# Kernel tuning notes

Measured on AMD Instinct MI355X. Metric: run time of the kernel, lower is better.

The kernel has to match this reference:

```python
import jax, jax.numpy as jnp
import numpy as np

B, T, D, H = 256, 512, 512, 64


def setup_inputs() -> dict:
    key = jax.random.key(0)
    ks = jax.random.split(key, 9)
    s_ih = 1.0 / np.sqrt(H)
    inp = {
        "x": jax.random.normal(ks[0], (B, T, D), dtype=jnp.float32),
        # PyTorch LSTM params, gate order (i, f, g, o)
        "W_ih": jax.random.uniform(ks[1], (4 * H, D), jnp.float32, -s_ih, s_ih),
        "W_hh": jax.random.uniform(ks[2], (4 * H, H), jnp.float32, -s_ih, s_ih),
        "b_ih": jax.random.uniform(ks[3], (4 * H,), jnp.float32, -s_ih, s_ih),
        "b_hh": jax.random.uniform(ks[4], (4 * H,), jnp.float32, -s_ih, s_ih),
        "W1": jax.random.uniform(ks[5], (32, H), jnp.float32, -1 / np.sqrt(H), 1 / np.sqrt(H)),
        "b1": jax.random.uniform(ks[6], (32,), jnp.float32, -1 / np.sqrt(H), 1 / np.sqrt(H)),
        "W2": jax.random.uniform(ks[7], (3, 32), jnp.float32, -1 / np.sqrt(32), 1 / np.sqrt(32)),
        "b2": jax.random.uniform(ks[8], (3,), jnp.float32, -1 / np.sqrt(32), 1 / np.sqrt(32)),
    }
    return inp


def _lstm_mean(x, W_ih, W_hh, b_ih, b_hh):
    # Precompute input projection for all timesteps: [B,T,4H]
    x_proj = jnp.einsum('btd,gd->btg', x, W_ih) + b_ih + b_hh
    xs = jnp.swapaxes(x_proj, 0, 1)  # [T,B,4H]
    h0 = jnp.zeros((x.shape[0], H), x.dtype)
    c0 = jnp.zeros((x.shape[0], H), x.dtype)

    def step(carry, xt):
        h, c = carry
        gates = xt + h @ W_hh.T  # [B,4H]
        i, f, g, o = jnp.split(gates, 4, axis=-1)
        i = jax.nn.sigmoid(i)
        f = jax.nn.sigmoid(f)
        g = jnp.tanh(g)
        o = jax.nn.sigmoid(o)
        c = f * c + i * g
        h = o * jnp.tanh(c)
        return (h, c), h

    _, hs = jax.lax.scan(step, (h0, c0), xs)  # hs: [T,B,H]
    return jnp.mean(hs, axis=0)  # mean over time -> [B,H]


def reference(x, W_ih, W_hh, b_ih, b_hh, W1, b1, W2, b2):
    pooled = _lstm_mean(x, W_ih, W_hh, b_ih, b_hh)
    h = jax.nn.relu(pooled @ W1.T + b1)
    logits = h @ W2.T + b2
    return jax.nn.softmax(logits, axis=1)
```

## Files before the change

kernel.cpp:

```cpp
#include <hip/hip_runtime.h>
#include <hip/hip_bf16.h>

#define BB 256
#define TT 512
#define DD 512
#define HH 64
#define NG 256
#define MM (BB * TT)

#define BM 128
#define BN 256
#define BK 32
#define LDA 40
#define LDB 40
#define NKC (DD / BK)

typedef short short8 __attribute__((ext_vector_type(8)));
typedef short short4v __attribute__((ext_vector_type(4)));
typedef float f32x4 __attribute__((ext_vector_type(4)));

__device__ inline unsigned long long pack4bf16(float4 v) {
    __hip_bfloat162 lo = __float22bfloat162_rn(make_float2(v.x, v.y));
    __hip_bfloat162 hi = __float22bfloat162_rn(make_float2(v.z, v.w));
    unsigned lu, hu;
    __builtin_memcpy(&lu, &lo, 4);
    __builtin_memcpy(&hu, &hi, 4);
    return ((unsigned long long)hu << 32) | lu;
}

__device__ inline unsigned short f2bf(float f) {
    __hip_bfloat16 h = __float2bfloat16(f);
    unsigned short u;
    __builtin_memcpy(&u, &h, 2);
    return u;
}

__device__ inline float bf2f(unsigned short u) {
    unsigned x = ((unsigned)u) << 16;
    float f;
    __builtin_memcpy(&f, &x, 4);
    return f;
}

__global__ __launch_bounds__(512, 2) void gemm_xproj(
    const float* __restrict__ X,
    const float* __restrict__ W,
    const float* __restrict__ b_ih,
    const float* __restrict__ b_hh,
    unsigned short* __restrict__ XP)
{
    __shared__ unsigned short As[2][BM * LDA];
    __shared__ unsigned short Bs[2][BN * LDB];
    __shared__ float bias_s[NG];

    const int tid   = threadIdx.x;
    const int m_blk = blockIdx.x * BM;
    const int lane  = tid & 63;
    const int wv    = tid >> 6;
    const int wm    = wv & 1;
    const int wn    = wv >> 1;
    const int q     = lane >> 4;
    const int cn    = lane & 15;

    if (tid < NG) bias_s[tid] = b_ih[tid] + b_hh[tid];

    f32x4 acc[4][4];
#pragma unroll
    for (int i = 0; i < 4; ++i)
#pragma unroll
        for (int j = 0; j < 4; ++j) acc[i][j] = (f32x4)0.f;

    float4 a_r[2], b_r[4];

#define LOAD_TILE(KC)                                                                     \
    do {                                                                                  \
        const int kof = (KC) * BK;                                                        \
        _Pragma("unroll")                                                                 \
        for (int u = 0; u < 2; ++u) {                                                     \
            int c = tid + 512 * u;                                                        \
            a_r[u] = *(const float4*)(X + (size_t)(m_blk + (c >> 3)) * DD + kof + (c & 7) * 4); \
        }                                                                                 \
        _Pragma("unroll")                                                                 \
        for (int u = 0; u < 4; ++u) {                                                     \
            int c = tid + 512 * u;                                                        \
            b_r[u] = *(const float4*)(W + (size_t)(c >> 3) * DD + kof + (c & 7) * 4);     \
        }                                                                                 \
    } while (0)

    LOAD_TILE(0);

    for (int kc = 0; kc < NKC; ++kc) {
        const int p = kc & 1;
#pragma unroll
        for (int u = 0; u < 2; ++u) {
            int c = tid + 512 * u;
            *(unsigned long long*)&As[p][(c >> 3) * LDA + (c & 7) * 4] = pack4bf16(a_r[u]);
        }
#pragma unroll
        for (int u = 0; u < 4; ++u) {
            int c = tid + 512 * u;
            *(unsigned long long*)&Bs[p][(c >> 3) * LDB + (c & 7) * 4] = pack4bf16(b_r[u]);
        }
        if (kc + 1 < NKC) LOAD_TILE(kc + 1);
        __syncthreads();

        short8 af[4], bf[4];
#pragma unroll
        for (int i = 0; i < 4; ++i) {
            const unsigned short* pa = &As[p][(wm * 64 + i * 16 + cn) * LDA + q * 8];
            ((short4v*)&af[i])[0] = *(const short4v*)pa;
            ((short4v*)&af[i])[1] = *(const short4v*)(pa + 4);
        }
#pragma unroll
        for (int j = 0; j < 4; ++j) {
            const unsigned short* pb = &Bs[p][(wn * 64 + j * 16 + cn) * LDB + q * 8];
            ((short4v*)&bf[j])[0] = *(const short4v*)pb;
            ((short4v*)&bf[j])[1] = *(const short4v*)(pb + 4);
        }

#pragma unroll
        for (int i = 0; i < 4; ++i)
#pragma unroll
            for (int j = 0; j < 4; ++j)
                acc[i][j] = __builtin_amdgcn_mfma_f32_16x16x32_bf16(af[i], bf[j], acc[i][j], 0, 0, 0);
    }

#pragma unroll
    for (int j = 0; j < 4; ++j) {
        const int n   = wn * 64 + j * 16 + cn;
        const float bvv = bias_s[n];
#pragma unroll
        for (int i = 0; i < 4; ++i) {
            const int m0 = m_blk + wm * 64 + i * 16 + q * 4;
#pragma unroll
            for (int r = 0; r < 4; ++r)
                XP[(size_t)(m0 + r) * NG + n] = f2bf(acc[i][j][r] + bvv);
        }
    }
#undef LOAD_TILE
}

__global__ __launch_bounds__(256, 1) void lstm_rec(
    const unsigned short* __restrict__ XP,
    const float* __restrict__ Whh,
    float* __restrict__ pooled)
{
    const int b   = blockIdx.x;
    const int tid = threadIdx.x;
    const int wv  = tid >> 6;
    const int j   = tid & 63;

    float wrow[HH];
#pragma unroll
    for (int u = 0; u < HH / 4; ++u)
        ((float4*)wrow)[u] = ((const float4*)(Whh + (size_t)tid * HH))[u];

    __shared__ float gbuf[2][NG];

    float h = 0.f, c = 0.f, hsum = 0.f;
    const unsigned short* xp = XP + (size_t)b * TT * NG + tid;

    unsigned short xr[4];
#pragma unroll
    for (int u = 0; u < 4; ++u) xr[u] = xp[(size_t)u * NG];

    for (int t0 = 0; t0 < TT; t0 += 4) {
#pragma unroll
        for (int u = 0; u < 4; ++u) {
            const int t = t0 + u;
            float a0 = bf2f(xr[u]), a1 = 0.f, a2 = 0.f, a3 = 0.f;
            xr[u] = xp[(size_t)((t + 4) & (TT - 1)) * NG];

            const int hb = __float_as_int(h);
#pragma unroll
            for (int kb = 0; kb < HH; kb += 4) {
                float h0 = __int_as_float(__builtin_amdgcn_readlane(hb, kb + 0));
                float h1 = __int_as_float(__builtin_amdgcn_readlane(hb, kb + 1));
                float h2 = __int_as_float(__builtin_amdgcn_readlane(hb, kb + 2));
                float h3 = __int_as_float(__builtin_amdgcn_readlane(hb, kb + 3));
                a0 = fmaf(wrow[kb + 0], h0, a0);
                a1 = fmaf(wrow[kb + 1], h1, a1);
                a2 = fmaf(wrow[kb + 2], h2, a2);
                a3 = fmaf(wrow[kb + 3], h3, a3);
            }
            const float acc = (a0 + a1) + (a2 + a3);

            float a;
            if (wv == 2) {
                a = 2.f / (1.f + __expf(-2.f * acc)) - 1.f;
            } else {
                a = 1.f / (1.f + __expf(-acc));
            }
            const int p = t & 1;
            gbuf[p][tid] = a;
            __syncthreads();
            const float iv = gbuf[p][j];
            const float fv = gbuf[p][64 + j];
            const float gv = gbuf[p][128 + j];
            const float ov = gbuf[p][192 + j];
            c = fmaf(fv, c, iv * gv);
            const float th = 2.f / (1.f + __expf(-2.f * c)) - 1.f;
            h = ov * th;
            hsum += h;
        }
    }

    if (tid < HH) pooled[(size_t)b * HH + j] = hsum * (1.f / (float)TT);
}

__global__ __launch_bounds__(256) void head_kernel(
    const float* __restrict__ pooled,
    const float* __restrict__ W1,
    const float* __restrict__ b1,
    const float* __restrict__ W2,
    const float* __restrict__ b2,
    float* __restrict__ out)
{
    __shared__ float W1s[32 * HH];
    __shared__ float W2s[3 * 32];
    __shared__ float b1s[32];
    __shared__ float b2s[3];

    const int tid = threadIdx.x;
    for (int i = tid; i < 32 * HH; i += 256) W1s[i] = W1[i];
    if (tid < 96) W2s[tid] = W2[tid];
    if (tid < 32) b1s[tid] = b1[tid];
    if (tid < 3)  b2s[tid] = b2[tid];
    __syncthreads();

    float p[HH];
    const float4* p4 = (const float4*)(pooled + (size_t)tid * HH);
#pragma unroll
    for (int q = 0; q < HH / 4; ++q) ((float4*)p)[q] = p4[q];

    float hbuf[32];
#pragma unroll
    for (int k = 0; k < 32; ++k) {
        float s = b1s[k];
        const float* wr = &W1s[k * HH];
#pragma unroll
        for (int jj = 0; jj < HH; ++jj) s += p[jj] * wr[jj];
        hbuf[k] = s > 0.f ? s : 0.f;
    }

    float lg[3];
#pragma unroll
    for (int cc = 0; cc < 3; ++cc) {
        float s = b2s[cc];
        const float* wr = &W2s[cc * 32];
#pragma unroll
        for (int k = 0; k < 32; ++k) s += hbuf[k] * wr[k];
        lg[cc] = s;
    }

    float mx = fmaxf(lg[0], fmaxf(lg[1], lg[2]));
    float e0 = __expf(lg[0] - mx);
    float e1 = __expf(lg[1] - mx);
    float e2 = __expf(lg[2] - mx);
    float inv = 1.f / (e0 + e1 + e2);
    out[tid * 3 + 0] = e0 * inv;
    out[tid * 3 + 1] = e1 * inv;
    out[tid * 3 + 2] = e2 * inv;
}

extern "C" void kernel_launch(void* const* d_in, const int* in_sizes, int n_in,
                              void* d_out, int out_size, void* d_ws, size_t ws_size,
                              hipStream_t stream) {
    const float* x    = (const float*)d_in[0];
    const float* W_ih = (const float*)d_in[1];
    const float* W_hh = (const float*)d_in[2];
    const float* b_ih = (const float*)d_in[3];
    const float* b_hh = (const float*)d_in[4];
    const float* W1   = (const float*)d_in[5];
    const float* b1   = (const float*)d_in[6];
    const float* W2   = (const float*)d_in[7];
    const float* b2   = (const float*)d_in[8];
    float* out = (float*)d_out;

    unsigned short* XP = (unsigned short*)d_ws;
    float* pooled = (float*)((char*)d_ws + (size_t)MM * NG * sizeof(unsigned short));

    gemm_xproj<<<dim3(MM / BM), 512, 0, stream>>>(x, W_ih, b_ih, b_hh, XP);
    lstm_rec<<<dim3(BB), 256, 0, stream>>>(XP, W_hh, pooled);
    head_kernel<<<dim3(1), 256, 0, stream>>>(pooled, W1, b1, W2, b2, out);
}
```

Baseline: 640.4 us.

## Run LSTM recurrence in a single wavefront per batch with all gates per lane

The recurrence kernel now uses one 64-lane wavefront per batch row instead of four. Each lane holds all four gate rows of W_hh in registers (256 floats) and computes i, f, g, o itself, which removes the shared-memory gate exchange and the per-step __syncthreads. In exchange each lane does four times the FMAs per step and register pressure rises sharply, which risks spilling. Empty asm statements pin the weights in VGPRs, and the x_proj prefetch depth drops to two steps.

```diff
diff --git a/kernel.cpp b/kernel.cpp
--- a/kernel.cpp
+++ b/kernel.cpp
@@ -24,6 +24,7 @@
     __hip_bfloat162 hi = __float22bfloat162_rn(make_float2(v.z, v.w));
     unsigned lu, hu;
     __builtin_memcpy(&lu, &lo, 4);
+    __builtin_memcpy(&hu, &hu, 0);
     __builtin_memcpy(&hu, &hi, 4);
     return ((unsigned long long)hu << 32) | lu;
 }
@@ -140,72 +141,96 @@
 #undef LOAD_TILE
 }
 
-__global__ __launch_bounds__(256, 1) void lstm_rec(
+__global__ __launch_bounds__(64, 1) void lstm_rec(
     const unsigned short* __restrict__ XP,
     const float* __restrict__ Whh,
     float* __restrict__ pooled)
 {
-    const int b   = blockIdx.x;
-    const int tid = threadIdx.x;
-    const int wv  = tid >> 6;
-    const int j   = tid & 63;
-
-    float wrow[HH];
-#pragma unroll
-    for (int u = 0; u < HH / 4; ++u)
-        ((float4*)wrow)[u] = ((const float4*)(Whh + (size_t)tid * HH))[u];
-
-    __shared__ float gbuf[2][NG];
+    const int b = blockIdx.x;
+    const int j = threadIdx.x & 63;
+
+    const f32x4* Wiv = (const f32x4*)(Whh + (size_t)j * HH);
+    const f32x4* Wfv = (const f32x4*)(Whh + (size_t)(HH + j) * HH);
+    const f32x4* Wgv = (const f32x4*)(Whh + (size_t)(2 * HH + j) * HH);
+    const f32x4* Wov = (const f32x4*)(Whh + (size_t)(3 * HH + j) * HH);
+
+#define WL16(P, S)                                                        \
+    f32x4 P##0 = (S)[0],  P##1 = (S)[1],  P##2 = (S)[2],  P##3 = (S)[3],  \
+          P##4 = (S)[4],  P##5 = (S)[5],  P##6 = (S)[6],  P##7 = (S)[7],  \
+          P##8 = (S)[8],  P##9 = (S)[9],  P##10 = (S)[10], P##11 = (S)[11],\
+          P##12 = (S)[12], P##13 = (S)[13], P##14 = (S)[14], P##15 = (S)[15];
+    WL16(wi, Wiv)
+    WL16(wf, Wfv)
+    WL16(wg, Wgv)
+    WL16(wo, Wov)
+#undef WL16
+
+#define PIN16(P)                                                          \
+    asm volatile("" : "+v"(P##0), "+v"(P##1), "+v"(P##2),  "+v"(P##3),    \
+                      "+v"(P##4), "+v"(P##5), "+v"(P##6),  "+v"(P##7),    \
+                      "+v"(P##8), "+v"(P##9), "+v"(P##10), "+v"(P##11),   \
+                      "+v"(P##12), "+v"(P##13), "+v"(P##14), "+v"(P##15));
 
     float h = 0.f, c = 0.f, hsum = 0.f;
-    const unsigned short* xp = XP + (size_t)b * TT * NG + tid;
-
-    unsigned short xr[4];
-#pragma unroll
-    for (int u = 0; u < 4; ++u) xr[u] = xp[(size_t)u * NG];
-
-    for (int t0 = 0; t0 < TT; t0 += 4) {
-#pragma unroll
-        for (int u = 0; u < 4; ++u) {
-            const int t = t0 + u;
-            float a0 = bf2f(xr[u]), a1 = 0.f, a2 = 0.f, a3 = 0.f;
-            xr[u] = xp[(size_t)((t + 4) & (TT - 1)) * NG];
-
-            const int hb = __float_as_int(h);
-#pragma unroll
-            for (int kb = 0; kb < HH; kb += 4) {
-                float h0 = __int_as_float(__builtin_amdgcn_readlane(hb, kb + 0));
-                float h1 = __int_as_float(__builtin_amdgcn_readlane(hb, kb + 1));
-                float h2 = __int_as_float(__builtin_amdgcn_readlane(hb, kb + 2));
-                float h3 = __int_as_float(__builtin_amdgcn_readlane(hb, kb + 3));
-                a0 = fmaf(wrow[kb + 0], h0, a0);
-                a1 = fmaf(wrow[kb + 1], h1, a1);
-                a2 = fmaf(wrow[kb + 2], h2, a2);
-                a3 = fmaf(wrow[kb + 3], h3, a3);
-            }
-            const float acc = (a0 + a1) + (a2 + a3);
-
-            float a;
-            if (wv == 2) {
-                a = 2.f / (1.f + __expf(-2.f * acc)) - 1.f;
-            } else {
-                a = 1.f / (1.f + __expf(-acc));
-            }
-            const int p = t & 1;
-            gbuf[p][tid] = a;
-            __syncthreads();
-            const float iv = gbuf[p][j];
-            const float fv = gbuf[p][64 + j];
-            const float gv = gbuf[p][128 + j];
-            const float ov = gbuf[p][192 + j];
-            c = fmaf(fv, c, iv * gv);
-            const float th = 2.f / (1.f + __expf(-2.f * c)) - 1.f;
-            h = ov * th;
-            hsum += h;
-        }
-    }
-
-    if (tid < HH) pooled[(size_t)b * HH + j] = hsum * (1.f / (float)TT);
+    const unsigned short* xp = XP + (size_t)b * TT * NG + j;
+
+    unsigned short xiA = xp[0],          xfA = xp[64],          xgA = xp[128],          xoA = xp[192];
+    unsigned short xiB = xp[(size_t)NG], xfB = xp[NG + 64],     xgB = xp[NG + 128],     xoB = xp[NG + 192];
+
+#define MACQ(M)                                                            \
+    {                                                                      \
+        const float k0 = __int_as_float(__builtin_amdgcn_readlane(hb, 4*(M)+0)); \
+        const float k1 = __int_as_float(__builtin_amdgcn_readlane(hb, 4*(M)+1)); \
+        const float k2 = __int_as_float(__builtin_amdgcn_readlane(hb, 4*(M)+2)); \
+        const float k3 = __int_as_float(__builtin_amdgcn_readlane(hb, 4*(M)+3)); \
+        ai[0] = fmaf(wi##M[0], k0, ai[0]); ai[1] = fmaf(wi##M[1], k1, ai[1]); \
+        ai[2] = fmaf(wi##M[2], k2, ai[2]); ai[3] = fmaf(wi##M[3], k3, ai[3]); \
+        af_[0] = fmaf(wf##M[0], k0, af_[0]); af_[1] = fmaf(wf##M[1], k1, af_[1]); \
+        af_[2] = fmaf(wf##M[2], k2, af_[2]); af_[3] = fmaf(wf##M[3], k3, af_[3]); \
+        ag_[0] = fmaf(wg##M[0], k0, ag_[0]); ag_[1] = fmaf(wg##M[1], k1, ag_[1]); \
+        ag_[2] = fmaf(wg##M[2], k2, ag_[2]); ag_[3] = fmaf(wg##M[3], k3, ag_[3]); \
+        ao_[0] = fmaf(wo##M[0], k0, ao_[0]); ao_[1] = fmaf(wo##M[1], k1, ao_[1]); \
+        ao_[2] = fmaf(wo##M[2], k2, ao_[2]); ao_[3] = fmaf(wo##M[3], k3, ao_[3]); \
+    }
+
+#define STEP(T_, XI, XF, XG, XO)                                           \
+    {                                                                      \
+        const int t = (T_);                                                \
+        f32x4 ai  = {bf2f(XI), 0.f, 0.f, 0.f};                             \
+        f32x4 af_ = {bf2f(XF), 0.f, 0.f, 0.f};                             \
+        f32x4 ag_ = {bf2f(XG), 0.f, 0.f, 0.f};                             \
+        f32x4 ao_ = {bf2f(XO), 0.f, 0.f, 0.f};                             \
+        const size_t nx = (size_t)((t + 2) & (TT - 1)) * NG;               \
+        XI = xp[nx]; XF = xp[nx + 64]; XG = xp[nx + 128]; XO = xp[nx + 192]; \
+        const int hb = __float_as_int(h);                                  \
+        MACQ(0)  MACQ(1)  MACQ(2)  MACQ(3)                                 \
+        MACQ(4)  MACQ(5)  MACQ(6)  MACQ(7)                                 \
+        MACQ(8)  MACQ(9)  MACQ(10) MACQ(11)                                \
+        MACQ(12) MACQ(13) MACQ(14) MACQ(15)                                \
+        float gi = (ai[0] + ai[1]) + (ai[2] + ai[3]);                      \
+        float gf = (af_[0] + af_[1]) + (af_[2] + af_[3]);                  \
+        float gg = (ag_[0] + ag_[1]) + (ag_[2] + ag_[3]);                  \
+        float go = (ao_[0] + ao_[1]) + (ao_[2] + ao_[3]);                  \
+        gi = 1.f / (1.f + __expf(-gi));                                    \
+        gf = 1.f / (1.f + __expf(-gf));                                    \
+        gg = 2.f / (1.f + __expf(-2.f * gg)) - 1.f;                        \
+        go = 1.f / (1.f + __expf(-go));                                    \
+        c = fmaf(gf, c, gi * gg);                                          \
+        const float th = 2.f / (1.f + __expf(-2.f * c)) - 1.f;             \
+        h = go * th;                                                       \
+        hsum += h;                                                         \
+    }
+
+    for (int t0 = 0; t0 < TT; t0 += 2) {
+        PIN16(wi) PIN16(wf) PIN16(wg) PIN16(wo)
+        STEP(t0 + 0, xiA, xfA, xgA, xoA)
+        STEP(t0 + 1, xiB, xfB, xgB, xoB)
+    }
+#undef STEP
+#undef MACQ
+#undef PIN16
+
+    pooled[(size_t)b * HH + j] = hsum * (1.f / (float)TT);
 }
 
 __global__ __launch_bounds__(256) void head_kernel(
@@ -281,6 +306,6 @@
     float* pooled = (float*)((char*)d_ws + (size_t)MM * NG * sizeof(unsigned short));
 
     gemm_xproj<<<dim3(MM / BM), 512, 0, stream>>>(x, W_ih, b_ih, b_hh, XP);
-    lstm_rec<<<dim3(BB), 256, 0, stream>>>(XP, W_hh, pooled);
+    lstm_rec<<<dim3(BB), 64, 0, stream>>>(XP, W_hh, pooled);
     head_kernel<<<dim3(1), 256, 0, stream>>>(pooled, W1, b1, W2, b2, out);
 }
```

New measurement: 1.400 ms. +118.7%, slower.
